# Kernel tuning notes

Hardware: AMD Instinct MI355X
Metric: run time of the kernel (lower is better)

The kernel has to match this reference:

```python
import jax, jax.numpy as jnp
import numpy as np

RADIUS = 0.2
NSAMPLE = 32
NPOINT = 2048
EPS = 1e-5


def setup_inputs() -> dict:
    key = jax.random.key(0)
    ks = jax.random.split(key, 6)
    B, N, C = 8, 8192, 64
    xyz = jax.random.uniform(ks[0], (B, N, 3), dtype=jnp.float32)
    features = jax.random.normal(ks[1], (B, C, N), dtype=jnp.float32)
    W1 = jax.random.normal(ks[2], (64, 67), dtype=jnp.float32) * 0.1
    W2 = jax.random.normal(ks[3], (64, 64), dtype=jnp.float32) * 0.1
    W3 = jax.random.normal(ks[4], (128, 64), dtype=jnp.float32) * 0.1
    return {
        'xyz': xyz, 'features': features,
        'W1': W1, 'g1': jnp.ones((64,), jnp.float32), 'b1': jnp.zeros((64,), jnp.float32),
        'W2': W2, 'g2': jnp.ones((64,), jnp.float32), 'b2': jnp.zeros((64,), jnp.float32),
        'W3': W3, 'g3': jnp.ones((128,), jnp.float32), 'b3': jnp.zeros((128,), jnp.float32),
    }


def furthest_point_sample(xyz, npoint):
    # xyz: (B, N, 3) -> (B, npoint) int32 indices, first index is 0 (CUDA FPS convention)
    B, N, _ = xyz.shape
    idxs0 = jnp.zeros((B, npoint), dtype=jnp.int32)
    dists0 = jnp.full((B, N), 1e10, dtype=xyz.dtype)
    last0 = jnp.zeros((B,), dtype=jnp.int32)

    def body(i, state):
        idxs, dists, last = state
        last_pt = xyz[jnp.arange(B), last]                      # (B, 3)
        d = jnp.sum((xyz - last_pt[:, None, :]) ** 2, axis=-1)  # (B, N)
        dists = jnp.minimum(dists, d)
        nxt = jnp.argmax(dists, axis=-1).astype(jnp.int32)
        idxs = idxs.at[:, i].set(nxt)
        return (idxs, dists, nxt)

    idxs, _, _ = jax.lax.fori_loop(1, npoint, body, (idxs0, dists0, last0))
    return idxs


def ball_query(xyz, new_xyz, radius, nsample):
    # Returns (B, S, nsample) int32: first `nsample` points within radius of each
    # query center, padded with the first in-ball index (pointnet2 convention).
    N = xyz.shape[1]
    d2 = jnp.sum((new_xyz[:, :, None, :] - xyz[:, None, :, :]) ** 2, axis=-1)  # (B,S,N)
    key = jnp.where(d2 < radius * radius, jnp.arange(N, dtype=jnp.int32), N)
    neg_vals, _ = jax.lax.top_k(-key, nsample)   # k smallest keys = earliest in-ball indices
    cand = -neg_vals                             # (B, S, nsample)
    first = cand[..., :1]
    return jnp.where(cand < N, cand, first)


def reference(xyz, features, W1, g1, b1, W2, g2, b2, W3, g3, b3):
    B = xyz.shape[0]
    fps_idx = furthest_point_sample(xyz, NPOINT)              # (B, S)
    new_xyz = xyz[jnp.arange(B)[:, None], fps_idx]            # (B, S, 3)

    idx = ball_query(xyz, new_xyz, RADIUS, NSAMPLE)           # (B, S, ns)
    bb = jnp.arange(B)[:, None, None]
    grouped_xyz = xyz[bb, idx] - new_xyz[:, :, None, :]       # (B, S, ns, 3) relative coords
    grouped_f = features.transpose(0, 2, 1)[bb, idx]          # (B, S, ns, C)
    g = jnp.concatenate([grouped_xyz, grouped_f], axis=-1)    # (B, S, ns, 3+C)
    g = g.transpose(0, 3, 1, 2)                               # (B, 3+C, S, ns)

    for W, ga, be in ((W1, g1, b1), (W2, g2, b2), (W3, g3, b3)):
        h = jnp.einsum('oc,bcsn->bosn', W, g)                 # 1x1 conv
        mu = h.mean(axis=(0, 2, 3), keepdims=True)            # training-mode BN stats
        var = h.var(axis=(0, 2, 3), keepdims=True)
        h = (h - mu) / jnp.sqrt(var + EPS)
        g = jax.nn.relu(h * ga[None, :, None, None] + be[None, :, None, None])

    feats = g.max(axis=-1)                                    # (B, mlp[-1], S)
    return new_xyz, feats
```

## Files before the change

### kernel.cpp

```cpp
#include <hip/hip_runtime.h>
#include <hip/hip_bf16.h>
#include <stdint.h>

#define NB 8
#define NN 8192
#define NC 64
#define NS 2048
#define NK 32
#define NCOL (NB*NS*NK)

typedef float v2f __attribute__((ext_vector_type(2)));

__device__ __forceinline__ unsigned short f2bf(float x) {
    union { float f; unsigned u; } c; c.f = x;
    unsigned r = c.u + 0x7fffu + ((c.u >> 16) & 1u);
    return (unsigned short)(r >> 16);
}
__device__ __forceinline__ float bf2f(unsigned v16) {
    union { float f; unsigned u; } c; c.u = v16 << 16;
    return c.f;
}

template<int CTRL>
__device__ __forceinline__ unsigned long long dpp_max_u64(unsigned long long key) {
    int olo = __builtin_amdgcn_update_dpp(0, (int)(unsigned)key,        CTRL, 0xf, 0xf, true);
    int ohi = __builtin_amdgcn_update_dpp(0, (int)(unsigned)(key >> 32), CTRL, 0xf, 0xf, true);
    unsigned long long ok = ((unsigned long long)(unsigned)ohi << 32) | (unsigned)olo;
    return ok > key ? ok : key;
}
template<int CTRL>
__device__ __forceinline__ float dpp_add_f32(float x) {
    int o = __builtin_amdgcn_update_dpp(0, __float_as_int(x), CTRL, 0xf, 0xf, true);
    return x + __int_as_float(o);
}
template<int CTRL>
__device__ __forceinline__ float dpp_max_f32(float x) {
    int o = __builtin_amdgcn_update_dpp(__float_as_int(x), __float_as_int(x), CTRL, 0xf, 0xf, false);
    return fmaxf(x, __int_as_float(o));
}
template<int CTRL>
__device__ __forceinline__ float dpp_min_f32(float x) {
    int o = __builtin_amdgcn_update_dpp(__float_as_int(x), __float_as_int(x), CTRL, 0xf, 0xf, false);
    return fminf(x, __int_as_float(o));
}
__device__ __forceinline__ float wave_red_min(float x) {
    x = dpp_min_f32<0x111>(x); x = dpp_min_f32<0x112>(x);
    x = dpp_min_f32<0x114>(x); x = dpp_min_f32<0x118>(x);
    x = dpp_min_f32<0x142>(x); x = dpp_min_f32<0x143>(x);
    return __int_as_float(__builtin_amdgcn_readlane(__float_as_int(x), 63));
}
__device__ __forceinline__ float wave_red_max(float x) {
    x = dpp_max_f32<0x111>(x); x = dpp_max_f32<0x112>(x);
    x = dpp_max_f32<0x114>(x); x = dpp_max_f32<0x118>(x);
    x = dpp_max_f32<0x142>(x); x = dpp_max_f32<0x143>(x);
    return __int_as_float(__builtin_amdgcn_readlane(__float_as_int(x), 63));
}
__device__ __forceinline__ v2f relu2(v2f v) {
    v.x = fmaxf(v.x, 0.f); v.y = fmaxf(v.y, 0.f); return v;
}

__device__ __forceinline__ unsigned expand_bits10(unsigned v) {
    v = (v * 0x00010001u) & 0xFF0000FFu;
    v = (v * 0x00000101u) & 0x0F00F00Fu;
    v = (v * 0x00000011u) & 0xC30C30C3u;
    v = (v * 0x00000005u) & 0x49249249u;
    return v;
}
__global__ __launch_bounds__(1024) void sort_kernel(const float* __restrict__ xyz,
    float4* __restrict__ sorted)
{
    __shared__ unsigned long long keys[NN];
    const int b = blockIdx.x;
    const int tid = threadIdx.x;
    const float* xb = xyz + (size_t)b * NN * 3;
    for (int p = tid; p < NN; p += 1024) {
        float x = xb[3*p+0], y = xb[3*p+1], z = xb[3*p+2];
        int qx = (int)(x * 1024.f); qx = qx < 0 ? 0 : (qx > 1023 ? 1023 : qx);
        int qy = (int)(y * 1024.f); qy = qy < 0 ? 0 : (qy > 1023 ? 1023 : qy);
        int qz = (int)(z * 1024.f); qz = qz < 0 ? 0 : (qz > 1023 ? 1023 : qz);
        unsigned m = expand_bits10((unsigned)qx)
                   | (expand_bits10((unsigned)qy) << 1)
                   | (expand_bits10((unsigned)qz) << 2);
        keys[p] = ((unsigned long long)m << 13) | (unsigned)p;
    }
    for (int k = 2; k <= NN; k <<= 1) {
        for (int j = k >> 1; j > 0; j >>= 1) {
            __syncthreads();
            for (int i = tid; i < NN; i += 1024) {
                int ixj = i ^ j;
                if (ixj > i) {
                    unsigned long long a = keys[i], c = keys[ixj];
                    bool up = ((i & k) == 0);
                    if ((a > c) == up) { keys[i] = c; keys[ixj] = a; }
                }
            }
        }
    }
    __syncthreads();
    for (int p = tid; p < NN; p += 1024) {
        int src = (int)(keys[p] & 0x1fffu);
        float4 v;
        v.x = xb[3*src+0]; v.y = xb[3*src+1]; v.z = xb[3*src+2];
        v.w = __int_as_float(src);
        sorted[(size_t)b * NN + p] = v;
    }
}

__global__ __launch_bounds__(1024) void fps_kernel(const float* __restrict__ xyz,
    const float4* __restrict__ sorted,
    float* __restrict__ new_xyz, float* __restrict__ out_newxyz)
{
#pragma clang fp contract(off)
    const int b = blockIdx.x;
    const int tid = threadIdx.x;
    const int w = tid >> 6;
    const int lane = tid & 63;
    __shared__ float sx[NN], sy[NN], sz[NN];
    __shared__ float s_hist[NS * 3];
    __shared__ unsigned long long s_key[16];
    const float4* sp = sorted + (size_t)b * NN + (size_t)w * 512 + lane;
    v2f px[4], py[4], pz[4], dmin[4];
    unsigned plo[8];
    float bnx = 1e30f, bny = 1e30f, bnz = 1e30f;
    float bxx = -1e30f, bxy = -1e30f, bxz = -1e30f;
#pragma unroll
    for (int m = 0; m < 4; ++m) {
        float4 a = sp[128*m];
        float4 c = sp[128*m + 64];
        px[m].x = a.x; px[m].y = c.x;
        py[m].x = a.y; py[m].y = c.y;
        pz[m].x = a.z; pz[m].y = c.z;
        dmin[m].x = 1e10f; dmin[m].y = 1e10f;
        int ia = __float_as_int(a.w), ic = __float_as_int(c.w);
        plo[2*m]   = ~(unsigned)ia;
        plo[2*m+1] = ~(unsigned)ic;
        sx[ia] = a.x; sy[ia] = a.y; sz[ia] = a.z;
        sx[ic] = c.x; sy[ic] = c.y; sz[ic] = c.z;
        bnx = fminf(bnx, fminf(a.x, c.x)); bxx = fmaxf(bxx, fmaxf(a.x, c.x));
        bny = fminf(bny, fminf(a.y, c.y)); bxy = fmaxf(bxy, fmaxf(a.y, c.y));
        bnz = fminf(bnz, fminf(a.z, c.z)); bxz = fmaxf(bxz, fmaxf(a.z, c.z));
    }
    bnx = wave_red_min(bnx); bny = wave_red_min(bny); bnz = wave_red_min(bnz);
    bxx = wave_red_max(bxx); bxy = wave_red_max(bxy); bxz = wave_red_max(bxz);

    const float* xb = xyz + (size_t)b * NN * 3;
    float lx = xb[0], ly = xb[1], lz = xb[2];
    if (tid == 0) { s_hist[0] = lx; s_hist[1] = ly; s_hist[2] = lz; }
    float ckv = 1e30f;
    unsigned cklo = 0u;
    __syncthreads();

    for (int i = 1; i < NS; ++i) {
        float cdx = fmaxf(fmaxf(bnx - lx, lx - bxx), 0.f);
        float cdy = fmaxf(fmaxf(bny - ly, ly - bxy), 0.f);
        float cdz = fmaxf(fmaxf(bnz - lz, lz - bxz), 0.f);
        float lb = (cdx*cdx + cdy*cdy) + cdz*cdz;
        if (!(lb >= ckv)) {
            v2f l2x; l2x.x = lx; l2x.y = lx;
            v2f l2y; l2y.x = ly; l2y.y = ly;
            v2f l2z; l2z.x = lz; l2z.y = lz;
            unsigned long long best = 0ull;
#pragma unroll
            for (int m = 0; m < 4; ++m) {
                v2f dx = px[m] - l2x;
                v2f dy = py[m] - l2y;
                v2f dz = pz[m] - l2z;
                v2f d = (dx*dx + dy*dy) + dz*dz;
                v2f dm;
                dm.x = fminf(dmin[m].x, d.x);
                dm.y = fminf(dmin[m].y, d.y);
                dmin[m] = dm;
                unsigned long long k0 =
                    ((unsigned long long)__float_as_uint(dm.x) << 32) | plo[2*m];
                unsigned long long k1 =
                    ((unsigned long long)__float_as_uint(dm.y) << 32) | plo[2*m+1];
                if (k0 > best) best = k0;
                if (k1 > best) best = k1;
            }
            best = dpp_max_u64<0x111>(best);
            best = dpp_max_u64<0x112>(best);
            best = dpp_max_u64<0x114>(best);
            best = dpp_max_u64<0x118>(best);
            best = dpp_max_u64<0x142>(best);
            best = dpp_max_u64<0x143>(best);
            ckv  = __uint_as_float((unsigned)__builtin_amdgcn_readlane((int)(best >> 32), 63));
            cklo = (unsigned)__builtin_amdgcn_readlane((int)(best & 0xffffffffull), 63);
        }
        if (lane == 0)
            s_key[w] = ((unsigned long long)__float_as_uint(ckv) << 32) | cklo;
        __syncthreads();
        if (w == 0) {
            unsigned long long k = s_key[lane & 15];
            k = dpp_max_u64<0x111>(k);
            k = dpp_max_u64<0x112>(k);
            k = dpp_max_u64<0x114>(k);
            k = dpp_max_u64<0x118>(k);
            int lo15 = __builtin_amdgcn_readlane((int)(k & 0xffffffffull), 15);
            int ix = ~lo15;
            float nx = sx[ix], ny = sy[ix], nz = sz[ix];
            if (lane == 0) {
                s_hist[3*i+0] = nx; s_hist[3*i+1] = ny; s_hist[3*i+2] = nz;
            }
        }
        __syncthreads();
        lx = s_hist[3*i+0]; ly = s_hist[3*i+1]; lz = s_hist[3*i+2];
    }
    float* nw = new_xyz + (size_t)b * NS * 3;
    float* ow = out_newxyz + (size_t)b * NS * 3;
    for (int t = tid; t < NS * 3; t += 1024) {
        float v = s_hist[t];
        nw[t] = v; ow[t] = v;
    }
}

__global__ __launch_bounds__(256) void transpose_kernel(const float* __restrict__ f,
    float* __restrict__ ft)
{
    __shared__ float tile[64][65];
    int b = blockIdx.y;
    int p0 = blockIdx.x * 64;
    for (int k = threadIdx.x; k < 64*64; k += 256) {
        int c = k >> 6, p = k & 63;
        tile[c][p] = f[((size_t)b * NC + c) * NN + p0 + p];
    }
    __syncthreads();
    for (int k = threadIdx.x; k < 64*64; k += 256) {
        int p = k >> 6, c = k & 63;
        ft[((size_t)b * NN + p0 + p) * NC + c] = tile[c][p];
    }
}

__global__ __launch_bounds__(256) void ballquery_kernel(const float* __restrict__ xyz,
    const float* __restrict__ new_xyz, int* __restrict__ idx)
{
#pragma clang fp contract(off)
    const int q = blockIdx.x * 4 + (threadIdx.x >> 6);
    const int lane = threadIdx.x & 63;
    const int b = q >> 11;
    const float r2 = (float)(0.2 * 0.2);
    const float* xb = xyz + (size_t)b * NN * 3;
    const float* nx = new_xyz + (size_t)q * 3;
    float qx = nx[0], qy = nx[1], qz = nx[2];
    int cnt = 0, first = -1;
    int* out = idx + (size_t)q * NK;
    for (int base = 0; base < NN; base += 64) {
        int p = base + lane;
        float x = xb[p*3+0], y = xb[p*3+1], z = xb[p*3+2];
        float dx = qx - x, dy = qy - y, dz = qz - z;
        float d2 = (dx*dx + dy*dy) + dz*dz;
        bool in = d2 < r2;
        unsigned long long m = __ballot(in);
        if (m) {
            if (first < 0) first = base + __builtin_ctzll(m);
            if (in) {
                int rank = cnt + __popcll(m & ((1ull << lane) - 1ull));
                if (rank < NK) out[rank] = p;
            }
            cnt += __popcll(m);
            if (cnt >= NK) break;
        }
    }
    for (int k = cnt + lane; k < NK; k += 64) out[k] = first;
}

__global__ __launch_bounds__(256, 2) void layer1_kernel(const float* __restrict__ xyz,
    const float* __restrict__ new_xyz, const int* __restrict__ idx,
    const float* __restrict__ ft, const float* __restrict__ W1,
    unsigned short* __restrict__ h1)
{
    const int col = blockIdx.x * 256 + threadIdx.x;
    const int b = col >> 16;
    const int s = (col >> 5) & 2047;
    const int p = idx[col];
    v2f g[34];
    float* gf = (float*)g;
    {
        const float* nx = new_xyz + ((size_t)(b * NS + s)) * 3;
        const float* xp = xyz + ((size_t)(b * NN + p)) * 3;
        gf[0] = xp[0] - nx[0]; gf[1] = xp[1] - nx[1]; gf[2] = xp[2] - nx[2];
    }
    const float4* fp = (const float4*)(ft + ((size_t)(b * NN + p)) * NC);
#pragma unroll
    for (int c4 = 0; c4 < 16; ++c4) {
        float4 v = fp[c4];
        gf[3 + 4*c4 + 0] = v.x; gf[3 + 4*c4 + 1] = v.y;
        gf[3 + 4*c4 + 2] = v.z; gf[3 + 4*c4 + 3] = v.w;
    }
    gf[67] = 0.f;
    uint4* dst = (uint4*)(h1 + (size_t)col * 64);
#pragma unroll
    for (int half = 0; half < 2; ++half) {
        float h[32];
#pragma unroll 4
        for (int o16 = 0; o16 < 32; ++o16) {
            const float* w = W1 + (half*32 + o16) * 67;
            v2f acc; acc.x = 0.f; acc.y = 0.f;
#pragma unroll
            for (int k = 0; k < 33; ++k) {
                v2f wv; wv.x = w[2*k]; wv.y = w[2*k+1];
                acc = wv * g[k] + acc;
            }
            h[o16] = fmaf(w[66], gf[66], acc.x + acc.y);
        }
#pragma unroll
        for (int k = 0; k < 4; ++k) {
            uint4 v;
            v.x = (unsigned)f2bf(h[8*k+0]) | ((unsigned)f2bf(h[8*k+1]) << 16);
            v.y = (unsigned)f2bf(h[8*k+2]) | ((unsigned)f2bf(h[8*k+3]) << 16);
            v.z = (unsigned)f2bf(h[8*k+4]) | ((unsigned)f2bf(h[8*k+5]) << 16);
            v.w = (unsigned)f2bf(h[8*k+6]) | ((unsigned)f2bf(h[8*k+7]) << 16);
            dst[half*4 + k] = v;
        }
    }
}

__global__ __launch_bounds__(256) void stats_kernel(const unsigned short* __restrict__ h,
    float* __restrict__ sums)
{
    __shared__ float ls[64], lq[64];
    const int tid = threadIdx.x;
    if (tid < 64) { ls[tid] = 0.f; lq[tid] = 0.f; }
    __syncthreads();
    float s[8] = {0,0,0,0,0,0,0,0}, q[8] = {0,0,0,0,0,0,0,0};
    const int gt = blockIdx.x * 256 + tid;
    const int G = gridDim.x * 256;
    const uint4* src = (const uint4*)h;
    const int nvec = NCOL * 8;
    for (int i = gt; i < nvec; i += G) {
        uint4 v = src[i];
        float f0 = bf2f(v.x & 0xffffu), f1 = bf2f(v.x >> 16);
        float f2 = bf2f(v.y & 0xffffu), f3 = bf2f(v.y >> 16);
        float f4 = bf2f(v.z & 0xffffu), f5 = bf2f(v.z >> 16);
        float f6 = bf2f(v.w & 0xffffu), f7 = bf2f(v.w >> 16);
        s[0] += f0; q[0] = fmaf(f0, f0, q[0]);
        s[1] += f1; q[1] = fmaf(f1, f1, q[1]);
        s[2] += f2; q[2] = fmaf(f2, f2, q[2]);
        s[3] += f3; q[3] = fmaf(f3, f3, q[3]);
        s[4] += f4; q[4] = fmaf(f4, f4, q[4]);
        s[5] += f5; q[5] = fmaf(f5, f5, q[5]);
        s[6] += f6; q[6] = fmaf(f6, f6, q[6]);
        s[7] += f7; q[7] = fmaf(f7, f7, q[7]);
    }
    const int obase = (tid & 7) * 8;
#pragma unroll
    for (int j = 0; j < 8; ++j) {
        atomicAdd(&ls[obase + j], s[j]);
        atomicAdd(&lq[obase + j], q[j]);
    }
    __syncthreads();
    if (tid < 64) {
        atomicAdd(&sums[tid*2+0], ls[tid]);
        atomicAdd(&sums[tid*2+1], lq[tid]);
    }
}

__global__ void finalize_kernel(const float* __restrict__ sums,
    const float* __restrict__ gamma, const float* __restrict__ beta,
    float* __restrict__ ab, int nch)
{
    int c = threadIdx.x;
    if (c < nch) {
        const float invM = 1.0f / 524288.0f;
        float mu = sums[c*2] * invM;
        float var = sums[c*2+1] * invM - mu * mu;
        float a = gamma[c] / sqrtf(var + 1e-5f);
        ab[c] = a;
        ab[nch + c] = fmaf(-mu, a, beta[c]);
    }
}

__global__ __launch_bounds__(256, 2) void layer2_kernel(const unsigned short* __restrict__ h1,
    const float* __restrict__ ab1, const float* __restrict__ W2,
    unsigned short* __restrict__ h2)
{
    const int col = blockIdx.x * 256 + threadIdx.x;
    const uint4* src = (const uint4*)(h1 + (size_t)col * 64);
    v2f g[32];
    float* gf = (float*)g;
#pragma unroll
    for (int k = 0; k < 8; ++k) {
        uint4 v = src[k];
        gf[8*k+0] = bf2f(v.x & 0xffffu); gf[8*k+1] = bf2f(v.x >> 16);
        gf[8*k+2] = bf2f(v.y & 0xffffu); gf[8*k+3] = bf2f(v.y >> 16);
        gf[8*k+4] = bf2f(v.z & 0xffffu); gf[8*k+5] = bf2f(v.z >> 16);
        gf[8*k+6] = bf2f(v.w & 0xffffu); gf[8*k+7] = bf2f(v.w >> 16);
    }
    const v2f* a2 = (const v2f*)ab1;
    const v2f* b2 = (const v2f*)(ab1 + 64);
#pragma unroll
    for (int k = 0; k < 32; ++k)
        g[k] = relu2(a2[k] * g[k] + b2[k]);
    uint4* dst = (uint4*)(h2 + (size_t)col * 64);
#pragma unroll
    for (int half = 0; half < 2; ++half) {
        float h[32];
#pragma unroll 4
        for (int o16 = 0; o16 < 32; ++o16) {
            const float* w = W2 + ((half*32 + o16) << 6);
            v2f acc; acc.x = 0.f; acc.y = 0.f;
#pragma unroll
            for (int k = 0; k < 32; ++k) {
                v2f wv; wv.x = w[2*k]; wv.y = w[2*k+1];
                acc = wv * g[k] + acc;
            }
            h[o16] = acc.x + acc.y;
        }
#pragma unroll
        for (int k = 0; k < 4; ++k) {
            uint4 v;
            v.x = (unsigned)f2bf(h[8*k+0]) | ((unsigned)f2bf(h[8*k+1]) << 16);
            v.y = (unsigned)f2bf(h[8*k+2]) | ((unsigned)f2bf(h[8*k+3]) << 16);
            v.z = (unsigned)f2bf(h[8*k+4]) | ((unsigned)f2bf(h[8*k+5]) << 16);
            v.w = (unsigned)f2bf(h[8*k+6]) | ((unsigned)f2bf(h[8*k+7]) << 16);
            dst[half*4 + k] = v;
        }
    }
}

__global__ __launch_bounds__(256, 2) void layer3_kernel(const unsigned short* __restrict__ h2,
    const float* __restrict__ ab2, const float* __restrict__ W3,
    float* __restrict__ hmax, float* __restrict__ hmin, float* __restrict__ sums3)
{
    __shared__ float ls[128], lq[128];
    const int tid = threadIdx.x;
    if (tid < 128) { ls[tid] = 0.f; lq[tid] = 0.f; }
    __syncthreads();
    const int col = blockIdx.x * 256 + tid;
    const int q = col >> 5;
    const uint4* src = (const uint4*)(h2 + (size_t)col * 64);
    v2f g[32];
    float* gf = (float*)g;
#pragma unroll
    for (int k = 0; k < 8; ++k) {
        uint4 v = src[k];
        gf[8*k+0] = bf2f(v.x & 0xffffu); gf[8*k+1] = bf2f(v.x >> 16);
        gf[8*k+2] = bf2f(v.y & 0xffffu); gf[8*k+3] = bf2f(v.y >> 16);
        gf[8*k+4] = bf2f(v.z & 0xffffu); gf[8*k+5] = bf2f(v.z >> 16);
        gf[8*k+6] = bf2f(v.w & 0xffffu); gf[8*k+7] = bf2f(v.w >> 16);
    }
    const v2f* a2 = (const v2f*)ab2;
    const v2f* b2 = (const v2f*)(ab2 + 64);
#pragma unroll
    for (int k = 0; k < 32; ++k)
        g[k] = relu2(a2[k] * g[k] + b2[k]);
    const bool leader = ((tid & 31) == 31);
#pragma unroll 2
    for (int o = 0; o < 128; ++o) {
        const float* w = W3 + (o << 6);
        v2f acc; acc.x = 0.f; acc.y = 0.f;
#pragma unroll
        for (int k = 0; k < 32; ++k) {
            v2f wv; wv.x = w[2*k]; wv.y = w[2*k+1];
            acc = wv * g[k] + acc;
        }
        float hv = acc.x + acc.y;
        float sm = hv, sq = hv*hv, mx = hv, mn = hv;
        sm = dpp_add_f32<0x111>(sm); sq = dpp_add_f32<0x111>(sq);
        mx = dpp_max_f32<0x111>(mx); mn = dpp_min_f32<0x111>(mn);
        sm = dpp_add_f32<0x112>(sm); sq = dpp_add_f32<0x112>(sq);
        mx = dpp_max_f32<0x112>(mx); mn = dpp_min_f32<0x112>(mn);
        sm = dpp_add_f32<0x114>(sm); sq = dpp_add_f32<0x114>(sq);
        mx = dpp_max_f32<0x114>(mx); mn = dpp_min_f32<0x114>(mn);
        sm = dpp_add_f32<0x118>(sm); sq = dpp_add_f32<0x118>(sq);
        mx = dpp_max_f32<0x118>(mx); mn = dpp_min_f32<0x118>(mn);
        sm = dpp_add_f32<0x142>(sm); sq = dpp_add_f32<0x142>(sq);
        mx = dpp_max_f32<0x142>(mx); mn = dpp_min_f32<0x142>(mn);
        if (leader) {
            hmax[(size_t)o * 16384 + q] = mx;
            hmin[(size_t)o * 16384 + q] = mn;
            atomicAdd(&ls[o], sm);
            atomicAdd(&lq[o], sq);
        }
    }
    __syncthreads();
    if (tid < 128) {
        atomicAdd(&sums3[tid*2+0], ls[tid]);
        atomicAdd(&sums3[tid*2+1], lq[tid]);
    }
}

__global__ __launch_bounds__(256) void final_kernel(const float* __restrict__ hmax,
    const float* __restrict__ hmin, const float* __restrict__ ab3,
    float* __restrict__ out)
{
    const int t = blockIdx.x * 256 + threadIdx.x;
    const int s = t & 2047;
    const int o = (t >> 11) & 127;
    const int b = t >> 18;
    const int q = (b << 11) + s;
    float a = ab3[o], c = ab3[128 + o];
    float h = (a >= 0.f) ? hmax[(size_t)o * 16384 + q] : hmin[(size_t)o * 16384 + q];
    out[t] = fmaxf(fmaf(a, h, c), 0.f);
}

extern "C" void kernel_launch(void* const* d_in, const int* in_sizes, int n_in,
                              void* d_out, int out_size, void* d_ws, size_t ws_size,
                              hipStream_t stream) {
    (void)in_sizes; (void)n_in; (void)out_size; (void)ws_size;
    const float* xyz      = (const float*)d_in[0];
    const float* features = (const float*)d_in[1];
    const float* W1 = (const float*)d_in[2];
    const float* g1 = (const float*)d_in[3];
    const float* b1 = (const float*)d_in[4];
    const float* W2 = (const float*)d_in[5];
    const float* g2 = (const float*)d_in[6];
    const float* b2 = (const float*)d_in[7];
    const float* W3 = (const float*)d_in[8];
    const float* g3 = (const float*)d_in[9];
    const float* b3 = (const float*)d_in[10];

    char* ws = (char*)d_ws;
    float*          new_xyz = (float*)(ws + 0);
    int*            idx     = (int*)(ws + 196608);
    float*          ft      = (float*)(ws + 2293760);
    unsigned short* h1      = (unsigned short*)(ws + 19070976);
    unsigned short* h2      = (unsigned short*)(ws + 86179840);
    float*          hmax    = (float*)(ws + 153288704);
    float*          hmin    = (float*)(ws + 161677312);
    float*          sums    = (float*)(ws + 170065920);
    float*          ab      = (float*)(ws + 170067968);
    float* sums1 = sums;        float* ab1 = ab;
    float* sums2 = sums + 128;  float* ab2 = ab + 128;
    float* sums3 = sums + 256;  float* ab3 = ab + 256;

    float4* sorted = (float4*)h1;

    float* out_newxyz = (float*)d_out;
    float* out_feats  = (float*)d_out + 49152;

    hipMemsetAsync(sums, 0, 2048, stream);

    sort_kernel<<<NB, 1024, 0, stream>>>(xyz, sorted);
    fps_kernel<<<NB, 1024, 0, stream>>>(xyz, sorted, new_xyz, out_newxyz);
    transpose_kernel<<<dim3(NN/64, NB), 256, 0, stream>>>(features, ft);
    ballquery_kernel<<<(NB*NS)/4, 256, 0, stream>>>(xyz, new_xyz, idx);
    layer1_kernel<<<NCOL/256, 256, 0, stream>>>(xyz, new_xyz, idx, ft, W1, h1);
    stats_kernel<<<1024, 256, 0, stream>>>(h1, sums1);
    finalize_kernel<<<1, 128, 0, stream>>>(sums1, g1, b1, ab1, 64);
    layer2_kernel<<<NCOL/256, 256, 0, stream>>>(h1, ab1, W2, h2);
    stats_kernel<<<1024, 256, 0, stream>>>(h2, sums2);
    finalize_kernel<<<1, 128, 0, stream>>>(sums2, g2, b2, ab2, 64);
    layer3_kernel<<<NCOL/256, 256, 0, stream>>>(h2, ab2, W3, hmax, hmin, sums3);
    finalize_kernel<<<1, 128, 0, stream>>>(sums3, g3, b3, ab3, 128);
    final_kernel<<<(NB*128*NS)/256, 256, 0, stream>>>(hmax, hmin, ab3, out_feats);
}
```

Baseline: 2.225 ms.

## Replace bitonic sort with counting sort and cut FPS to one barrier per step

The full bitonic sort of Morton keys is replaced by a counting sort over the top 11 Morton bits, using a shared-memory histogram, a DPP prefix scan and atomic scatter. In FPS, every wave now does the 16-way cross-wave reduction redundantly, and the per-wave key slot is double-buffered by iteration parity, which removes the second __syncthreads per step. The 64-bit argmax is split into a float max reduction plus an index max among ties. Point order within a bucket becomes nondeterministic, which only changes the pruning layout, and each wave now reads the three shared coordinates every iteration.

Result: no change. 2.261 ms (+1.6%).

```diff
diff --git a/kernel.cpp b/kernel.cpp
--- a/kernel.cpp
+++ b/kernel.cpp
@@ -43,6 +43,17 @@
     int o = __builtin_amdgcn_update_dpp(__float_as_int(x), __float_as_int(x), CTRL, 0xf, 0xf, false);
     return fminf(x, __int_as_float(o));
 }
+template<int CTRL>
+__device__ __forceinline__ unsigned dpp_max_u32(unsigned x) {
+    int o = __builtin_amdgcn_update_dpp((int)x, (int)x, CTRL, 0xf, 0xf, false);
+    unsigned ou = (unsigned)o;
+    return x > ou ? x : ou;
+}
+template<int CTRL, int RM>
+__device__ __forceinline__ unsigned dpp_add_u32(unsigned x) {
+    int o = __builtin_amdgcn_update_dpp(0, (int)x, CTRL, RM, 0xf, true);
+    return x + (unsigned)o;
+}
 __device__ __forceinline__ float wave_red_min(float x) {
     x = dpp_min_f32<0x111>(x); x = dpp_min_f32<0x112>(x);
     x = dpp_min_f32<0x114>(x); x = dpp_min_f32<0x118>(x);
@@ -69,10 +80,16 @@
 __global__ __launch_bounds__(1024) void sort_kernel(const float* __restrict__ xyz,
     float4* __restrict__ sorted)
 {
-    __shared__ unsigned long long keys[NN];
+    __shared__ unsigned cnt[2048];
+    __shared__ unsigned codes[NN];
+    __shared__ unsigned wsum[16];
     const int b = blockIdx.x;
     const int tid = threadIdx.x;
+    const int w = tid >> 6;
+    const int lane = tid & 63;
     const float* xb = xyz + (size_t)b * NN * 3;
+    cnt[tid] = 0; cnt[tid + 1024] = 0;
+    __syncthreads();
     for (int p = tid; p < NN; p += 1024) {
         float x = xb[3*p+0], y = xb[3*p+1], z = xb[3*p+2];
         int qx = (int)(x * 1024.f); qx = qx < 0 ? 0 : (qx > 1023 ? 1023 : qx);
@@ -81,28 +98,39 @@
         unsigned m = expand_bits10((unsigned)qx)
                    | (expand_bits10((unsigned)qy) << 1)
                    | (expand_bits10((unsigned)qz) << 2);
-        keys[p] = ((unsigned long long)m << 13) | (unsigned)p;
-    }
-    for (int k = 2; k <= NN; k <<= 1) {
-        for (int j = k >> 1; j > 0; j >>= 1) {
-            __syncthreads();
-            for (int i = tid; i < NN; i += 1024) {
-                int ixj = i ^ j;
-                if (ixj > i) {
-                    unsigned long long a = keys[i], c = keys[ixj];
-                    bool up = ((i & k) == 0);
-                    if ((a > c) == up) { keys[i] = c; keys[ixj] = a; }
-                }
-            }
-        }
-    }
+        unsigned bk = m >> 19;
+        codes[p] = bk;
+        atomicAdd(&cnt[bk], 1u);
+    }
+    __syncthreads();
+    unsigned c0 = cnt[2*tid], c1 = cnt[2*tid+1];
+    unsigned s = c0 + c1;
+    unsigned v = s;
+    v = dpp_add_u32<0x111, 0xf>(v);
+    v = dpp_add_u32<0x112, 0xf>(v);
+    v = dpp_add_u32<0x114, 0xf>(v);
+    v = dpp_add_u32<0x118, 0xf>(v);
+    v = dpp_add_u32<0x142, 0xa>(v);
+    v = dpp_add_u32<0x143, 0xc>(v);
+    if (lane == 63) wsum[w] = v;
+    __syncthreads();
+    unsigned wbase = 0;
+#pragma unroll
+    for (int j = 0; j < 15; ++j) {
+        unsigned t = wsum[j];
+        wbase += (j < w) ? t : 0u;
+    }
+    unsigned excl = wbase + v - s;
+    cnt[2*tid]   = excl;
+    cnt[2*tid+1] = excl + c0;
     __syncthreads();
     for (int p = tid; p < NN; p += 1024) {
-        int src = (int)(keys[p] & 0x1fffu);
-        float4 v;
-        v.x = xb[3*src+0]; v.y = xb[3*src+1]; v.z = xb[3*src+2];
-        v.w = __int_as_float(src);
-        sorted[(size_t)b * NN + p] = v;
+        unsigned bk = codes[p];
+        unsigned pos = atomicAdd(&cnt[bk], 1u);
+        float4 o;
+        o.x = xb[3*p+0]; o.y = xb[3*p+1]; o.z = xb[3*p+2];
+        o.w = __int_as_float(p);
+        sorted[(size_t)b * NN + pos] = o;
     }
 }
 
@@ -117,7 +145,7 @@
     const int lane = tid & 63;
     __shared__ float sx[NN], sy[NN], sz[NN];
     __shared__ float s_hist[NS * 3];
-    __shared__ unsigned long long s_key[16];
+    __shared__ unsigned long long s_key[2][16];
     const float4* sp = sorted + (size_t)b * NN + (size_t)w * 512 + lane;
     v2f px[4], py[4], pz[4], dmin[4];
     unsigned plo[8];
@@ -159,52 +187,53 @@
             v2f l2x; l2x.x = lx; l2x.y = lx;
             v2f l2y; l2y.x = ly; l2y.y = ly;
             v2f l2z; l2z.x = lz; l2z.y = lz;
-            unsigned long long best = 0ull;
 #pragma unroll
             for (int m = 0; m < 4; ++m) {
                 v2f dx = px[m] - l2x;
                 v2f dy = py[m] - l2y;
                 v2f dz = pz[m] - l2z;
                 v2f d = (dx*dx + dy*dy) + dz*dz;
-                v2f dm;
-                dm.x = fminf(dmin[m].x, d.x);
-                dm.y = fminf(dmin[m].y, d.y);
-                dmin[m] = dm;
-                unsigned long long k0 =
-                    ((unsigned long long)__float_as_uint(dm.x) << 32) | plo[2*m];
-                unsigned long long k1 =
-                    ((unsigned long long)__float_as_uint(dm.y) << 32) | plo[2*m+1];
-                if (k0 > best) best = k0;
-                if (k1 > best) best = k1;
+                dmin[m].x = fminf(dmin[m].x, d.x);
+                dmin[m].y = fminf(dmin[m].y, d.y);
             }
-            best = dpp_max_u64<0x111>(best);
-            best = dpp_max_u64<0x112>(best);
-            best = dpp_max_u64<0x114>(best);
-            best = dpp_max_u64<0x118>(best);
-            best = dpp_max_u64<0x142>(best);
-            best = dpp_max_u64<0x143>(best);
-            ckv  = __uint_as_float((unsigned)__builtin_amdgcn_readlane((int)(best >> 32), 63));
-            cklo = (unsigned)__builtin_amdgcn_readlane((int)(best & 0xffffffffull), 63);
+            float bv = fmaxf(
+                fmaxf(fmaxf(dmin[0].x, dmin[0].y), fmaxf(dmin[1].x, dmin[1].y)),
+                fmaxf(fmaxf(dmin[2].x, dmin[2].y), fmaxf(dmin[3].x, dmin[3].y)));
+            float mv = bv;
+            mv = dpp_max_f32<0x111>(mv); mv = dpp_max_f32<0x112>(mv);
+            mv = dpp_max_f32<0x114>(mv); mv = dpp_max_f32<0x118>(mv);
+            mv = dpp_max_f32<0x142>(mv); mv = dpp_max_f32<0x143>(mv);
+            const unsigned vmb = (unsigned)__builtin_amdgcn_readlane(__float_as_int(mv), 63);
+            const float vmax = __uint_as_float(vmb);
+            unsigned cand = 0u;
+#pragma unroll
+            for (int m = 0; m < 4; ++m) {
+                unsigned t0 = (dmin[m].x == vmax) ? plo[2*m]   : 0u;
+                unsigned t1 = (dmin[m].y == vmax) ? plo[2*m+1] : 0u;
+                unsigned t = t0 > t1 ? t0 : t1;
+                cand = cand > t ? cand : t;
+            }
+            cand = dpp_max_u32<0x111>(cand); cand = dpp_max_u32<0x112>(cand);
+            cand = dpp_max_u32<0x114>(cand); cand = dpp_max_u32<0x118>(cand);
+            cand = dpp_max_u32<0x142>(cand); cand = dpp_max_u32<0x143>(cand);
+            cklo = (unsigned)__builtin_amdgcn_readlane((int)cand, 63);
+            ckv = vmax;
         }
         if (lane == 0)
-            s_key[w] = ((unsigned long long)__float_as_uint(ckv) << 32) | cklo;
+            s_key[i & 1][w] = ((unsigned long long)__float_as_uint(ckv) << 32) | cklo;
         __syncthreads();
-        if (w == 0) {
-            unsigned long long k = s_key[lane & 15];
-            k = dpp_max_u64<0x111>(k);
-            k = dpp_max_u64<0x112>(k);
-            k = dpp_max_u64<0x114>(k);
-            k = dpp_max_u64<0x118>(k);
-            int lo15 = __builtin_amdgcn_readlane((int)(k & 0xffffffffull), 15);
-            int ix = ~lo15;
-            float nx = sx[ix], ny = sy[ix], nz = sz[ix];
-            if (lane == 0) {
-                s_hist[3*i+0] = nx; s_hist[3*i+1] = ny; s_hist[3*i+2] = nz;
-            }
-        }
-        __syncthreads();
-        lx = s_hist[3*i+0]; ly = s_hist[3*i+1]; lz = s_hist[3*i+2];
-    }
+        unsigned long long k = s_key[i & 1][lane & 15];
+        k = dpp_max_u64<0x111>(k);
+        k = dpp_max_u64<0x112>(k);
+        k = dpp_max_u64<0x114>(k);
+        k = dpp_max_u64<0x118>(k);
+        const int ix = ~__builtin_amdgcn_readlane((int)(unsigned)(k & 0xffffffffull), 15);
+        lx = sx[ix]; ly = sy[ix]; lz = sz[ix];
+        if (tid == 0) {
+            s_hist[3*i+0] = lx; s_hist[3*i+1] = ly; s_hist[3*i+2] = lz;
+        }
+    }
+    __syncthreads();
     float* nw = new_xyz + (size_t)b * NS * 3;
     float* ow = out_newxyz + (size_t)b * NS * 3;
     for (int t = tid; t < NS * 3; t += 1024) {
```

## Replace bitonic Morton sort with counting-sort bucketing by top Morton bits

Applied to the files above, without the earlier changes.

The per-batch bitonic sort of 64-bit Morton keys in shared memory is replaced with a counting sort on the top 11 bits of the Morton code. It uses shared-memory atomics for a histogram, a DPP-based prefix scan, and an atomic scatter. This removes the roughly 91 synchronized compare-exchange passes, at the cost of only approximate spatial ordering within buckets and a nondeterministic order inside each bucket. The FPS consumer relies on the sorted layout and carries the original index in .w, so correctness should hold, though FPS locality may change slightly.

Measured after the change: 2.112 ms. 1.05x faster.

```diff
diff --git a/kernel.cpp b/kernel.cpp
--- a/kernel.cpp
+++ b/kernel.cpp
@@ -43,6 +43,11 @@
     int o = __builtin_amdgcn_update_dpp(__float_as_int(x), __float_as_int(x), CTRL, 0xf, 0xf, false);
     return fminf(x, __int_as_float(o));
 }
+template<int CTRL, int RM>
+__device__ __forceinline__ unsigned dpp_add_u32(unsigned x) {
+    int o = __builtin_amdgcn_update_dpp(0, (int)x, CTRL, RM, 0xf, true);
+    return x + (unsigned)o;
+}
 __device__ __forceinline__ float wave_red_min(float x) {
     x = dpp_min_f32<0x111>(x); x = dpp_min_f32<0x112>(x);
     x = dpp_min_f32<0x114>(x); x = dpp_min_f32<0x118>(x);
@@ -69,10 +74,16 @@
 __global__ __launch_bounds__(1024) void sort_kernel(const float* __restrict__ xyz,
     float4* __restrict__ sorted)
 {
-    __shared__ unsigned long long keys[NN];
+    __shared__ unsigned cnt[2048];
+    __shared__ unsigned codes[NN];
+    __shared__ unsigned wsum[16];
     const int b = blockIdx.x;
     const int tid = threadIdx.x;
+    const int w = tid >> 6;
+    const int lane = tid & 63;
     const float* xb = xyz + (size_t)b * NN * 3;
+    cnt[tid] = 0; cnt[tid + 1024] = 0;
+    __syncthreads();
     for (int p = tid; p < NN; p += 1024) {
         float x = xb[3*p+0], y = xb[3*p+1], z = xb[3*p+2];
         int qx = (int)(x * 1024.f); qx = qx < 0 ? 0 : (qx > 1023 ? 1023 : qx);
@@ -81,28 +92,39 @@
         unsigned m = expand_bits10((unsigned)qx)
                    | (expand_bits10((unsigned)qy) << 1)
                    | (expand_bits10((unsigned)qz) << 2);
-        keys[p] = ((unsigned long long)m << 13) | (unsigned)p;
-    }
-    for (int k = 2; k <= NN; k <<= 1) {
-        for (int j = k >> 1; j > 0; j >>= 1) {
-            __syncthreads();
-            for (int i = tid; i < NN; i += 1024) {
-                int ixj = i ^ j;
-                if (ixj > i) {
-                    unsigned long long a = keys[i], c = keys[ixj];
-                    bool up = ((i & k) == 0);
-                    if ((a > c) == up) { keys[i] = c; keys[ixj] = a; }
-                }
-            }
-        }
-    }
+        unsigned bk = m >> 19;
+        codes[p] = bk;
+        atomicAdd(&cnt[bk], 1u);
+    }
+    __syncthreads();
+    unsigned c0 = cnt[2*tid], c1 = cnt[2*tid+1];
+    unsigned s = c0 + c1;
+    unsigned v = s;
+    v = dpp_add_u32<0x111, 0xf>(v);
+    v = dpp_add_u32<0x112, 0xf>(v);
+    v = dpp_add_u32<0x114, 0xf>(v);
+    v = dpp_add_u32<0x118, 0xf>(v);
+    v = dpp_add_u32<0x142, 0xa>(v);
+    v = dpp_add_u32<0x143, 0xc>(v);
+    if (lane == 63) wsum[w] = v;
+    __syncthreads();
+    unsigned wbase = 0;
+#pragma unroll
+    for (int j = 0; j < 15; ++j) {
+        unsigned t = wsum[j];
+        wbase += (j < w) ? t : 0u;
+    }
+    unsigned excl = wbase + v - s;
+    cnt[2*tid]   = excl;
+    cnt[2*tid+1] = excl + c0;
     __syncthreads();
     for (int p = tid; p < NN; p += 1024) {
-        int src = (int)(keys[p] & 0x1fffu);
-        float4 v;
-        v.x = xb[3*src+0]; v.y = xb[3*src+1]; v.z = xb[3*src+2];
-        v.w = __int_as_float(src);
-        sorted[(size_t)b * NN + p] = v;
+        unsigned bk = codes[p];
+        unsigned pos = atomicAdd(&cnt[bk], 1u);
+        float4 o;
+        o.x = xb[3*p+0]; o.y = xb[3*p+1]; o.z = xb[3*p+2];
+        o.w = __int_as_float(p);
+        sorted[(size_t)b * NN + pos] = o;
     }
 }
 
@@ -205,6 +227,7 @@
         __syncthreads();
         lx = s_hist[3*i+0]; ly = s_hist[3*i+1]; lz = s_hist[3*i+2];
     }
+    __syncthreads();
     float* nw = new_xyz + (size_t)b * NS * 3;
     float* ow = out_newxyz + (size_t)b * NS * 3;
     for (int t = tid; t < NS * 3; t += 1024) {
```
